# Kernel optimization log

Hardware: AMD Instinct MI355X
Metric: run time of the kernel (lower is better)

Reference implementation:

```python
import jax, jax.numpy as jnp
import numpy as np

N_GRAMS = 3
N_KERNELS = 11

def _kernel_mus(K):
    l = [1.0]
    if K == 1:
        return l
    bs = 2.0 / (K - 1)
    l.append(1.0 - bs / 2.0)
    for i in range(1, K - 1):
        l.append(l[i] - bs)
    return l

def _kernel_sigmas(K):
    if K == 1:
        return [0.001]
    bs = 2.0 / (K - 1)
    return [0.001] + [0.5 * bs] * (K - 1)

MU = jnp.asarray(_kernel_mus(N_KERNELS), jnp.float32)       # (K,)
SIGMA = jnp.asarray(_kernel_sigmas(N_KERNELS), jnp.float32)  # (K,)

def _conv_relu(x, w, b):
    # x: (B,E,L), w: (O,E,h); right-pad h-1 so output length == L (as ConstantPad1d((0,h-1)))
    h = w.shape[-1]
    y = jax.lax.conv_general_dilated(x, w, (1,), [(0, h - 1)], dimension_numbers=('NCH', 'OIH', 'NCH'))
    return jax.nn.relu(y + b[None, :, None]).transpose(0, 2, 1)  # (B,L,O)

def _cosine(a, b):
    # CosineMatrixAttention: normalize rows then matmul
    an = a / (jnp.linalg.norm(a, axis=-1, keepdims=True) + 1e-13)
    bn = b / (jnp.linalg.norm(b, axis=-1, keepdims=True) + 1e-13)
    return jnp.einsum('bqe,bde->bqd', an, bn)

def setup_inputs() -> dict:
    key = jax.random.key(0)
    ks = jax.random.split(key, 12)
    B, Lq, Ld, V, E, O = 128, 64, 512, 30000, 300, 128
    inp = {}
    inp['tokens_q'] = jax.random.randint(ks[0], (B, Lq), 0, V)
    inp['tokens_d'] = jax.random.randint(ks[1], (B, Ld), 0, V)
    inp['emb'] = jax.random.normal(ks[2], (V, E), jnp.float32) * 0.1
    for i, h in enumerate((1, 2, 3)):
        inp['conv_w%d' % h] = jax.random.normal(ks[3 + i], (O, E, h), jnp.float32) * (1.0 / np.sqrt(E * h))
        inp['conv_b%d' % h] = jnp.zeros((O,), jnp.float32)
    inp['fc_w'] = jax.random.normal(ks[9], (1, N_KERNELS * N_GRAMS * N_GRAMS), jnp.float32) * 0.1
    inp['fc_b'] = jnp.zeros((1,), jnp.float32)
    return inp

def reference(tokens_q, tokens_d, emb, conv_w1, conv_b1, conv_w2, conv_b2, conv_w3, conv_b3, fc_w, fc_b):
    qmask = (tokens_q > 0).astype(jnp.float32)  # (B,Lq)
    dmask = (tokens_d > 0).astype(jnp.float32)  # (B,Ld)
    qe = emb[tokens_q].transpose(0, 2, 1)  # (B,E,Lq)
    de = emb[tokens_d].transpose(0, 2, 1)  # (B,E,Ld)
    cws = [(conv_w1, conv_b1), (conv_w2, conv_b2), (conv_w3, conv_b3)]
    hq = [_conv_relu(qe, w, b) for w, b in cws]  # each (B,Lq,O)
    hd = [_conv_relu(de, w, b) for w, b in cws]  # each (B,Ld,O)
    pair_mask = qmask[:, :, None] * dmask[:, None, :]  # (B,Lq,Ld)
    mu = MU[None, None, None, :]
    sig = SIGMA[None, None, None, :]
    feats = []
    for q in range(N_GRAMS):
        for d in range(N_GRAMS):
            m = _cosine(hq[q], hd[d]) * pair_mask  # (B,Lq,Ld)
            rbf = jnp.exp(-jnp.square(m[..., None] - mu) / (2.0 * jnp.square(sig))) * pair_mask[..., None]
            qk = rbf.sum(axis=2)  # (B,Lq,K)
            logk = jnp.log(jnp.maximum(qk, 1e-10)) * 0.01
            # NOTE: original has a typo (loq_ vs log_) so the query mask is NOT applied before summing
            feats.append(logk.sum(axis=1))  # (B,K)
    cross = jnp.concatenate(feats, axis=-1)  # (B, K*G*G)
    return cross @ fc_w.T + fc_b  # (B,1)
```

## Files before the change

### kernel.cpp

```cpp
#include <hip/hip_runtime.h>
#include <hip/hip_bf16.h>

typedef __attribute__((ext_vector_type(8))) short short8;
typedef __attribute__((ext_vector_type(4))) float f32x4;
typedef __attribute__((ext_vector_type(2))) unsigned int u32x2;

#define E_DIM 300
#define NCH   128
#define NOUT  384
#define NCHUNK 30

#define OPITCH 792

__device__ __forceinline__ unsigned short f2bf(float f) {
    unsigned int u = __float_as_uint(f);
    u += 0x7FFFu + ((u >> 16) & 1u);
    return (unsigned short)(u >> 16);
}

__device__ __forceinline__ void xcd_map(int bx, int& b, int& p) {
    int x = bx & 7;
    int j = bx >> 3;
    b = x * 16 + j / 9;
    p = j - (j / 9) * 9;
}

__global__ void pack_wb(const float* __restrict__ w1, const float* __restrict__ w2,
                        const float* __restrict__ w3, unsigned short* __restrict__ Wp) {
    int idx = blockIdx.x * 256 + threadIdx.x;
    if (idx >= NCHUNK * NOUT * 32) return;
    int ke = idx & 31;
    int n  = (idx >> 5) % NOUT;
    int c  = idx / (32 * NOUT);
    int s  = c / 10;
    int e  = (c % 10) * 32 + ke;
    int g  = n >> 7, o = n & 127, h = g + 1;
    float v = 0.0f;
    if (e < E_DIM && s < h) {
        const float* w = (g == 0) ? w1 : ((g == 1) ? w2 : w3);
        v = w[(o * E_DIM + e) * h + s];
    }
    Wp[idx] = f2bf(v);
}

__global__ void pack_emb(const float* __restrict__ emb, unsigned short* __restrict__ embh) {
    int u = blockIdx.x * 256 + threadIdx.x;
    if (u >= 30000 * 40) return;
    int row = u / 40;
    int c8  = u - row * 40;
    int col = c8 * 8;
    ushort4 lo = {0, 0, 0, 0}, hi = {0, 0, 0, 0};
    const float* src = emb + (size_t)row * E_DIM + col;
    if (col + 8 <= E_DIM) {
        float4 a = *(const float4*)src;
        float4 c = *(const float4*)(src + 4);
        lo.x = f2bf(a.x); lo.y = f2bf(a.y); lo.z = f2bf(a.z); lo.w = f2bf(a.w);
        hi.x = f2bf(c.x); hi.y = f2bf(c.y); hi.z = f2bf(c.z); hi.w = f2bf(c.w);
    } else if (col < E_DIM) {
        float4 a = *(const float4*)src;
        lo.x = f2bf(a.x); lo.y = f2bf(a.y); lo.z = f2bf(a.z); lo.w = f2bf(a.w);
    }
    unsigned short* dst = embh + (size_t)row * 320 + col;
    *(ushort4*)dst       = lo;
    *(ushort4*)(dst + 4) = hi;
}

__launch_bounds__(512, 4)
__global__ void conv_mfma(const int* __restrict__ tokens_q, const int* __restrict__ tokens_d,
                          const unsigned short* __restrict__ embh, const unsigned short* __restrict__ Wp,
                          const float* __restrict__ b1, const float* __restrict__ b2,
                          const float* __restrict__ b3,
                          unsigned short* __restrict__ hq, unsigned short* __restrict__ hd) {
    __shared__ __align__(16) char lds[64 * OPITCH];
    __shared__ float nrm[64 * 3];

    int b, tile;
    xcd_map(blockIdx.x, b, tile);
    int isq  = (tile == 0);
    int L    = isq ? 64 : 512;
    int t0   = isq ? 0 : (tile - 1) * 64;
    const int* toks = isq ? (tokens_q + b * 64) : (tokens_d + b * 512);
    int tid  = threadIdx.x;
    int lane = tid & 63;
    int wn   = tid >> 6;
    int lr   = lane & 15;
    int lg   = lane >> 4;

    if (tid < 192) nrm[tid] = 0.0f;

    const unsigned short* __restrict__ wpB = Wp + (size_t)(wn * 16 + lr) * 32 + lg * 8;
    short8 bb[2][3];
    #pragma unroll
    for (int g = 0; g < 3; ++g) {
        bb[0][g] = *(const short8*)(wpB + (size_t)(0 * NOUT + g * 128) * 32);
        bb[1][g] = *(const short8*)(wpB + (size_t)(1 * NOUT + g * 128) * 32);
    }

    {
        auto gather_row = [&](int r, int sl) {
            int pos = t0 + r;
            int tk  = (pos < L) ? toks[pos] : -1;
            char* wbase = lds + r * 640;
            int xr = (r & 7) << 4;
            if (tk >= 0) {
                const unsigned short* src = embh + (size_t)tk * 320 + sl * 8;
                uint4 v[5];
                #pragma unroll
                for (int k = 0; k < 5; ++k) v[k] = *(const uint4*)(src + k * 64);
                #pragma unroll
                for (int k = 0; k < 5; ++k)
                    *(uint4*)(wbase + (((sl + 8 * k) * 16) ^ xr)) = v[k];
            } else {
                uint4 z = {0, 0, 0, 0};
                #pragma unroll
                for (int k = 0; k < 5; ++k)
                    *(uint4*)(wbase + (((sl + 8 * k) * 16) ^ xr)) = z;
            }
        };
        gather_row(tid >> 3, tid & 7);
        if (tid < 16) gather_row(64 + (tid >> 3), tid & 7);
    }
    __syncthreads();

    f32x4 acc[4][3];
    #pragma unroll
    for (int i = 0; i < 4; ++i)
        #pragma unroll
        for (int g = 0; g < 3; ++g) acc[i][g] = (f32x4){0.f, 0.f, 0.f, 0.f};

    #pragma unroll
    for (int c = 0; c < NCHUNK; ++c) {
        const int S  = (c >= 20) ? 2 : ((c >= 10) ? 1 : 0);
        const int ec = c - S * 10;
        short8 a[4];
        #pragma unroll
        for (int i = 0; i < 4; ++i) {
            int row = i * 16 + lr + S;
            int byt = (ec * 64 + lg * 16) ^ ((row & 7) << 4);
            a[i] = *(const short8*)(lds + row * 640 + byt);
        }
        #pragma unroll
        for (int i = 0; i < 4; ++i)
            #pragma unroll
            for (int g = S; g < 3; ++g)
                acc[i][g] = __builtin_amdgcn_mfma_f32_16x16x32_bf16(a[i], bb[c & 1][g], acc[i][g], 0, 0, 0);
        if (c < NCHUNK - 2) {
            const int S2 = ((c + 2) >= 20) ? 2 : (((c + 2) >= 10) ? 1 : 0);
            #pragma unroll
            for (int g = S2; g < 3; ++g)
                bb[c & 1][g] = *(const short8*)(wpB + (size_t)((c + 2) * NOUT + g * 128) * 32);
        }
    }

    #pragma unroll
    for (int g = 0; g < 3; ++g) {
        float bv = (g == 0 ? b1 : (g == 1 ? b2 : b3))[wn * 16 + lr];
        #pragma unroll
        for (int i = 0; i < 4; ++i)
            #pragma unroll
            for (int r = 0; r < 4; ++r) {
                float v = acc[i][g][r] + bv;
                v = v > 0.0f ? v : 0.0f;
                acc[i][g][r] = v;
                float s = v * v;
                s += __shfl_xor(s, 1, 16);
                s += __shfl_xor(s, 2, 16);
                s += __shfl_xor(s, 4, 16);
                s += __shfl_xor(s, 8, 16);
                if (lr == 0) atomicAdd(&nrm[(i * 16 + lg * 4 + r) * 3 + g], s);
            }
    }
    __syncthreads();

    if (tid < 192) nrm[tid] = 1.0f / (sqrtf(nrm[tid]) + 1e-13f);
    __syncthreads();

    unsigned short* os = (unsigned short*)lds;
    #pragma unroll
    for (int i = 0; i < 4; ++i)
        #pragma unroll
        for (int r = 0; r < 4; ++r) {
            int row = i * 16 + lg * 4 + r;
            #pragma unroll
            for (int g = 0; g < 3; ++g)
                os[row * (OPITCH / 2) + g * 128 + wn * 16 + lr] = f2bf(acc[i][g][r] * nrm[row * 3 + g]);
        }
    __syncthreads();

    unsigned short* outp = isq ? hq : hd;
    #pragma unroll
    for (int it = 0; it < 12; ++it) {
        int idx = it * 512 + tid;
        int row = idx / 96;
        int c8  = idx - row * 96;
        int g   = c8 >> 5;
        int ch  = (c8 & 31) * 4;
        u32x2 v = *(const u32x2*)(lds + row * OPITCH + c8 * 8);
        __builtin_nontemporal_store(v, (u32x2*)&outp[((size_t)(g * 128 + b) * L + t0 + row) * NCH + ch]);
    }
}

#define DPITCH 136
__launch_bounds__(256, 3)
__global__ void sim_rbf(const unsigned short* __restrict__ hq,
                        const unsigned short* __restrict__ hd,
                        const int* __restrict__ tokens_q, const int* __restrict__ tokens_d,
                        float* __restrict__ cross) {
    __shared__ __align__(16) short ds2[2][64 * DPITCH];
    __shared__ unsigned char dm_s[512];
    __shared__ float logk_s[11];

    int b, p;
    xcd_map(blockIdx.x, b, p);
    int gq = p / 3;
    int gd = p % 3;
    int tid = threadIdx.x;
    int lane = tid & 63;
    int wn   = tid >> 6;
    int lr   = lane & 15;
    int lg   = lane >> 4;

    if (tid < 11) logk_s[tid] = 0.0f;

    const unsigned short* qsrc = hq + ((size_t)(gq * 128 + b) * 64) * NCH;
    const unsigned short* dsrc = hd + ((size_t)(gd * 128 + b) * 512) * NCH;

    int q  = wn * 16 + lr;

    short8 qf[4];
    #pragma unroll
    for (int ks = 0; ks < 4; ++ks)
        qf[ks] = *(const short8*)&qsrc[q * NCH + ks * 32 + lg * 8];
    float qm = (tokens_q[b * 64 + q] > 0) ? 1.0f : 0.0f;

    int srow  = tid >> 4;
    int scol8 = (tid & 15) * 8;

    {
        uint4 s4[4];
        #pragma unroll
        for (int it = 0; it < 4; ++it)
            s4[it] = *(const uint4*)&dsrc[(size_t)(it * 16 + srow) * NCH + scol8];
        for (int i = tid; i < 512; i += 256)
            dm_s[i] = (tokens_d[b * 512 + i] > 0) ? 1 : 0;
        #pragma unroll
        for (int it = 0; it < 4; ++it)
            *(uint4*)&ds2[0][(it * 16 + srow) * DPITCH + scol8] = s4[it];
    }
    __syncthreads();

    float qk[11];
    #pragma unroll
    for (int k = 0; k < 11; ++k) qk[k] = 0.0f;

    const float C4 = 0.0183156389f;

    for (int ch = 0; ch < 8; ++ch) {
        int buf = ch & 1;
        uint4 r4[4];
        if (ch < 7) {
            #pragma unroll
            for (int it = 0; it < 4; ++it)
                r4[it] = *(const uint4*)&dsrc[((size_t)(ch + 1) * 64 + it * 16 + srow) * NCH + scol8];
        }

        #pragma unroll
        for (int mt = 0; mt < 4; ++mt) {
            f32x4 acc = (f32x4){0.f, 0.f, 0.f, 0.f};
            #pragma unroll
            for (int ks = 0; ks < 4; ++ks) {
                short8 a = *(const short8*)&ds2[buf][(mt * 16 + lr) * DPITCH + ks * 32 + lg * 8];
                acc = __builtin_amdgcn_mfma_f32_16x16x32_bf16(a, qf[ks], acc, 0, 0, 0);
            }
            uchar4 du = *(const uchar4*)&dm_s[ch * 64 + mt * 16 + lg * 4];
            float cv[4], cm[4];
            cm[0] = qm * (float)du.x; cm[1] = qm * (float)du.y;
            cm[2] = qm * (float)du.z; cm[3] = qm * (float)du.w;
            #pragma unroll
            for (int r = 0; r < 4; ++r) cv[r] = acc[r] * cm[r];

            float cmx = fmaxf(fmaxf(cv[0], cv[1]), fmaxf(cv[2], cv[3]));
            if (__any(cmx > 0.98f)) {
                #pragma unroll
                for (int r = 0; r < 4; ++r) {
                    if (cv[r] > 0.98f) {
                        float t0 = cv[r] - 1.0f;
                        qk[0] += __expf(-500000.0f * t0 * t0);
                    }
                }
            }
            #pragma unroll
            for (int r = 0; r < 4; ++r) {
                float c  = cv[r];
                float tA = c - 0.1f;
                float TA = __expf(-50.0f * tA * tA) * cm[r];
                float UA = __expf(20.0f * c - 4.0f);
                float tB = c + 0.1f;
                float TB = __expf(-50.0f * tB * tB) * cm[r];
                float UB = __expf(-20.0f * c - 4.0f);
                qk[5] += TA;
                TA *= UA; qk[4] += TA; UA *= C4;
                TA *= UA; qk[3] += TA; UA *= C4;
                TA *= UA; qk[2] += TA; UA *= C4;
                TA *= UA; qk[1] += TA;
                qk[6] += TB;
                TB *= UB; qk[7] += TB; UB *= C4;
                TB *= UB; qk[8] += TB; UB *= C4;
                TB *= UB; qk[9] += TB; UB *= C4;
                TB *= UB; qk[10] += TB;
            }
        }

        if (ch < 7) {
            #pragma unroll
            for (int it = 0; it < 4; ++it)
                *(uint4*)&ds2[buf ^ 1][(it * 16 + srow) * DPITCH + scol8] = r4[it];
        }
        __syncthreads();
    }

    #pragma unroll
    for (int k = 0; k < 11; ++k) {
        float v = qk[k];
        v += __shfl_xor(v, 16);
        v += __shfl_xor(v, 32);
        qk[k] = v;
    }
    if (lg == 0) {
        #pragma unroll
        for (int k = 0; k < 11; ++k) {
            float lv = __logf(fmaxf(qk[k], 1e-10f)) * 0.01f;
            atomicAdd(&logk_s[k], lv);
        }
    }
    __syncthreads();
    if (tid < 11) cross[b * 99 + p * 11 + tid] = logk_s[tid];
}

__global__ void fc_kernel(const float* __restrict__ cross, const float* __restrict__ fc_w,
                          const float* __restrict__ fc_b, float* __restrict__ out) {
    int b = threadIdx.x;
    float acc = fc_b[0];
    #pragma unroll 11
    for (int j = 0; j < 99; ++j) acc += cross[b * 99 + j] * fc_w[j];
    out[b] = acc;
}

extern "C" void kernel_launch(void* const* d_in, const int* in_sizes, int n_in,
                              void* d_out, int out_size, void* d_ws, size_t ws_size,
                              hipStream_t stream) {
    const int*   tq  = (const int*)d_in[0];
    const int*   td  = (const int*)d_in[1];
    const float* emb = (const float*)d_in[2];
    const float* w1  = (const float*)d_in[3];
    const float* cb1 = (const float*)d_in[4];
    const float* w2  = (const float*)d_in[5];
    const float* cb2 = (const float*)d_in[6];
    const float* w3  = (const float*)d_in[7];
    const float* cb3 = (const float*)d_in[8];
    const float* fcw = (const float*)d_in[9];
    const float* fcb = (const float*)d_in[10];

    char* ws = (char*)d_ws;
    unsigned short* Wp    = (unsigned short*)ws;
    float*          cross = (float*)(ws + 921600);
    unsigned short* hq    = (unsigned short*)(ws + 1048576);
    unsigned short* hd    = (unsigned short*)(ws + 8388608);
    unsigned short* embh  = (unsigned short*)(ws + 58720256);

    hipLaunchKernelGGL(pack_wb, dim3(1440), dim3(256), 0, stream, w1, w2, w3, Wp);
    hipLaunchKernelGGL(pack_emb, dim3(4688), dim3(256), 0, stream, emb, embh);
    hipLaunchKernelGGL(conv_mfma, dim3(128 * 9), dim3(512), 0, stream,
                       tq, td, embh, Wp, cb1, cb2, cb3, hq, hd);
    hipLaunchKernelGGL(sim_rbf, dim3(128 * 9), dim3(256), 0, stream, hq, hd, tq, td, cross);
    hipLaunchKernelGGL(fc_kernel, dim3(1), dim3(128), 0, stream, cross, fcw, fcb, (float*)d_out);
}
```

Before: 183.7 us.

## Stage document tiles with direct global-to-LDS loads and XOR-swizzled layout

Result: faster. 175.8 us (-4.3%).

```diff
diff --git a/kernel.cpp b/kernel.cpp
--- a/kernel.cpp
+++ b/kernel.cpp
@@ -11,6 +11,10 @@
 #define NCHUNK 30
 
 #define OPITCH 792
+
+#define GLD16(gp, lp) __builtin_amdgcn_global_load_lds( \
+    (const __attribute__((address_space(1))) unsigned int*)(const void*)(gp), \
+    (__attribute__((address_space(3))) unsigned int*)(void*)(lp), 16, 0, 0)
 
 __device__ __forceinline__ unsigned short f2bf(float f) {
     unsigned int u = __float_as_uint(f);
@@ -200,13 +204,12 @@
     }
 }
 
-#define DPITCH 136
-__launch_bounds__(256, 3)
+__launch_bounds__(256, 2)
 __global__ void sim_rbf(const unsigned short* __restrict__ hq,
                         const unsigned short* __restrict__ hd,
                         const int* __restrict__ tokens_q, const int* __restrict__ tokens_d,
                         float* __restrict__ cross) {
-    __shared__ __align__(16) short ds2[2][64 * DPITCH];
+    __shared__ __align__(16) short ds2[2][64 * 128];
     __shared__ unsigned char dm_s[512];
     __shared__ float logk_s[11];
 
@@ -226,27 +229,21 @@
     const unsigned short* dsrc = hd + ((size_t)(gd * 128 + b) * 512) * NCH;
 
     int q  = wn * 16 + lr;
-
-    short8 qf[4];
-    #pragma unroll
-    for (int ks = 0; ks < 4; ++ks)
-        qf[ks] = *(const short8*)&qsrc[q * NCH + ks * 32 + lg * 8];
     float qm = (tokens_q[b * 64 + q] > 0) ? 1.0f : 0.0f;
 
-    int srow  = tid >> 4;
-    int scol8 = (tid & 15) * 8;
-
-    {
-        uint4 s4[4];
+    int rloc = 4 * wn + (lane >> 4);
+    int cu   = (lane & 15) ^ (rloc & 7);
+
+    auto stage = [&](int bufI, int ch) {
+        const unsigned short* s0 = dsrc + ((size_t)ch * 64 + rloc) * NCH + cu * 8;
         #pragma unroll
         for (int it = 0; it < 4; ++it)
-            s4[it] = *(const uint4*)&dsrc[(size_t)(it * 16 + srow) * NCH + scol8];
-        for (int i = tid; i < 512; i += 256)
-            dm_s[i] = (tokens_d[b * 512 + i] > 0) ? 1 : 0;
-        #pragma unroll
-        for (int it = 0; it < 4; ++it)
-            *(uint4*)&ds2[0][(it * 16 + srow) * DPITCH + scol8] = s4[it];
-    }
+            GLD16(s0 + (size_t)it * 16 * NCH, &ds2[bufI][(it * 16 + 4 * wn) * 128]);
+    };
+
+    stage(0, 0);
+    for (int i = tid; i < 512; i += 256)
+        dm_s[i] = (tokens_d[b * 512 + i] > 0) ? 1 : 0;
     __syncthreads();
 
     float qk[11];
@@ -257,19 +254,21 @@
 
     for (int ch = 0; ch < 8; ++ch) {
         int buf = ch & 1;
-        uint4 r4[4];
-        if (ch < 7) {
-            #pragma unroll
-            for (int it = 0; it < 4; ++it)
-                r4[it] = *(const uint4*)&dsrc[((size_t)(ch + 1) * 64 + it * 16 + srow) * NCH + scol8];
-        }
+        if (ch < 7) stage(buf ^ 1, ch + 1);
+
+        short8 qf[4];
+        #pragma unroll
+        for (int ks = 0; ks < 4; ++ks)
+            qf[ks] = *(const short8*)&qsrc[q * NCH + ks * 32 + lg * 8];
 
         #pragma unroll
         for (int mt = 0; mt < 4; ++mt) {
+            int r = mt * 16 + lr;
             f32x4 acc = (f32x4){0.f, 0.f, 0.f, 0.f};
             #pragma unroll
             for (int ks = 0; ks < 4; ++ks) {
-                short8 a = *(const short8*)&ds2[buf][(mt * 16 + lr) * DPITCH + ks * 32 + lg * 8];
+                short8 a = *(const short8*)((const char*)&ds2[buf][0]
+                              + r * 256 + (((ks * 4 + lg) ^ (r & 7)) << 4));
                 acc = __builtin_amdgcn_mfma_f32_16x16x32_bf16(a, qf[ks], acc, 0, 0, 0);
             }
             uchar4 du = *(const uchar4*)&dm_s[ch * 64 + mt * 16 + lg * 4];
@@ -277,26 +276,26 @@
             cm[0] = qm * (float)du.x; cm[1] = qm * (float)du.y;
             cm[2] = qm * (float)du.z; cm[3] = qm * (float)du.w;
             #pragma unroll
-            for (int r = 0; r < 4; ++r) cv[r] = acc[r] * cm[r];
+            for (int r2 = 0; r2 < 4; ++r2) cv[r2] = acc[r2] * cm[r2];
 
             float cmx = fmaxf(fmaxf(cv[0], cv[1]), fmaxf(cv[2], cv[3]));
             if (__any(cmx > 0.98f)) {
                 #pragma unroll
-                for (int r = 0; r < 4; ++r) {
-                    if (cv[r] > 0.98f) {
-                        float t0 = cv[r] - 1.0f;
+                for (int r2 = 0; r2 < 4; ++r2) {
+                    if (cv[r2] > 0.98f) {
+                        float t0 = cv[r2] - 1.0f;
                         qk[0] += __expf(-500000.0f * t0 * t0);
                     }
                 }
             }
             #pragma unroll
-            for (int r = 0; r < 4; ++r) {
-                float c  = cv[r];
+            for (int r2 = 0; r2 < 4; ++r2) {
+                float c  = cv[r2];
                 float tA = c - 0.1f;
-                float TA = __expf(-50.0f * tA * tA) * cm[r];
+                float TA = __expf(-50.0f * tA * tA) * cm[r2];
                 float UA = __expf(20.0f * c - 4.0f);
                 float tB = c + 0.1f;
-                float TB = __expf(-50.0f * tB * tB) * cm[r];
+                float TB = __expf(-50.0f * tB * tB) * cm[r2];
                 float UB = __expf(-20.0f * c - 4.0f);
                 qk[5] += TA;
                 TA *= UA; qk[4] += TA; UA *= C4;
@@ -311,11 +310,6 @@
             }
         }
 
-        if (ch < 7) {
-            #pragma unroll
-            for (int it = 0; it < 4; ++it)
-                *(uint4*)&ds2[buf ^ 1][(it * 16 + srow) * DPITCH + scol8] = r4[it];
-        }
         __syncthreads();
     }
 
```
